# Performance work log

Measured on AMD Instinct MI355X. Metric: run time of the kernel, lower is better.

## Reference

```python
import jax, jax.numpy as jnp
import numpy as np

DIM = 1024
HEADS = 16
HEAD_DIM = DIM // HEADS  # 64
EPS = 1e-5


def layer_norm(x, w, b):
    # LayerNorm over last dim (head_dim), matching nn.LayerNorm defaults
    mu = jnp.mean(x, axis=-1, keepdims=True)
    var = jnp.mean(jnp.square(x - mu), axis=-1, keepdims=True)
    return (x - mu) * jax.lax.rsqrt(var + EPS) * w + b


def apply_rotary_emb(x, freqs):
    # x: [B, S, H, D]; freqs: [S, D/2] angles. Interleaved (complex) rotary:
    # pairs (x[2i], x[2i+1]) rotated by angle freqs[:, i].
    x1 = x[..., 0::2]
    x2 = x[..., 1::2]
    cos = jnp.cos(freqs)[None, :, None, :]
    sin = jnp.sin(freqs)[None, :, None, :]
    r1 = x1 * cos - x2 * sin
    r2 = x1 * sin + x2 * cos
    return jnp.stack([r1, r2], axis=-1).reshape(x.shape)


def setup_inputs() -> dict:
    key = jax.random.key(0)
    ks = jax.random.split(key, 8)
    B, S = 2, 2048
    x = jax.random.normal(ks[0], (B, S, DIM), dtype=jnp.float32)
    freqs = jax.random.uniform(ks[1], (S, HEAD_DIM // 2), dtype=jnp.float32)
    sc = 1.0 / np.sqrt(DIM)
    w_qkv = jax.random.normal(ks[2], (DIM, 4 * DIM), dtype=jnp.float32) * sc
    w_out = jax.random.normal(ks[3], (DIM, DIM), dtype=jnp.float32) * sc
    qn_w = jnp.ones((HEAD_DIM,), jnp.float32)
    qn_b = jnp.zeros((HEAD_DIM,), jnp.float32)
    kn_w = jnp.ones((HEAD_DIM,), jnp.float32)
    kn_b = jnp.zeros((HEAD_DIM,), jnp.float32)
    return {"x": x, "freqs": freqs, "w_qkv": w_qkv, "w_out": w_out,
            "qn_w": qn_w, "qn_b": qn_b, "kn_w": kn_w, "kn_b": kn_b}


def reference(x, freqs, w_qkv, w_out, qn_w, qn_b, kn_w, kn_b):
    B, S, _ = x.shape
    qkv = x @ w_qkv  # [B, S, 4*DIM]
    q, k, v, gate = jnp.split(qkv, 4, axis=-1)
    q = q.reshape(B, S, HEADS, HEAD_DIM)
    k = k.reshape(B, S, HEADS, HEAD_DIM)
    v = v.reshape(B, S, HEADS, HEAD_DIM)
    q = layer_norm(q, qn_w, qn_b)
    k = layer_norm(k, kn_w, kn_b)
    q = apply_rotary_emb(q, freqs)
    k = apply_rotary_emb(k, freqs)
    # flash_attn_func: non-causal softmax attention, scale 1/sqrt(head_dim)
    scale = 1.0 / np.sqrt(HEAD_DIM)
    scores = jnp.einsum('bqhd,bkhd->bhqk', q, k) * scale
    probs = jax.nn.softmax(scores, axis=-1)
    o = jnp.einsum('bhqk,bkhd->bqhd', probs, v)
    o = o.reshape(B, S, DIM)
    o = o * jax.nn.sigmoid(gate)
    return o @ w_out
```

## Files before the change

### kernel.cpp

```cpp
#include <hip/hip_runtime.h>


typedef _Float16 f16;
typedef _Float16 f16x8 __attribute__((ext_vector_type(8)));
typedef _Float16 f16x4 __attribute__((ext_vector_type(4)));
typedef float    f32x4 __attribute__((ext_vector_type(4)));

#define MFMA16(a, b, c) __builtin_amdgcn_mfma_f32_16x16x32_f16((a), (b), (c), 0, 0, 0)

__device__ __forceinline__ void gload16(const void* g, void* l) {
  __builtin_amdgcn_global_load_lds(
      (const __attribute__((address_space(1))) void*)g,
      (__attribute__((address_space(3))) void*)l, 16, 0, 0);
}

__device__ __forceinline__ float exp2_fast(float x) {
#if __has_builtin(__builtin_amdgcn_exp2f)
  return __builtin_amdgcn_exp2f(x);
#else
  float r;
  asm("v_exp_f32 %0, %1" : "=v"(r) : "v"(x));
  return r;
#endif
}
__device__ __forceinline__ unsigned pkrtz(float a, float b) {
  typedef __fp16 hf16x2 __attribute__((ext_vector_type(2)));
  union { hf16x2 h; unsigned u; } c;
  c.h = __builtin_amdgcn_cvt_pkrtz(a, b);
  return c.u;
}

__global__ void rope_table_kernel(const float* __restrict__ freqs, float* __restrict__ tbl) {
  int i = blockIdx.x * 256 + threadIdx.x;
  if (i >= 2048 * 32) return;
  int s = i >> 5, j = i & 31;
  float f = freqs[i];
  tbl[s * 64 + j]      = cosf(f);
  tbl[s * 64 + 32 + j] = sinf(f);
}

__global__ void cast_f16_kernel(const float* __restrict__ in, f16* __restrict__ out, int n8) {
  int i = blockIdx.x * 256 + threadIdx.x;
  if (i >= n8) return;
  float4 a = ((const float4*)in)[2 * i];
  float4 b = ((const float4*)in)[2 * i + 1];
  f16x8 o;
  o[0] = (f16)a.x; o[1] = (f16)a.y; o[2] = (f16)a.z; o[3] = (f16)a.w;
  o[4] = (f16)b.x; o[5] = (f16)b.y; o[6] = (f16)b.z; o[7] = (f16)b.w;
  ((f16x8*)out)[i] = o;
}

__global__ void transpose_cast_kernel(const float* __restrict__ in, f16* __restrict__ out,
                                      int R, int C) {
  __shared__ float t[64][65];
  int c0 = blockIdx.x * 64, r0 = blockIdx.y * 64;
  int tx = threadIdx.x & 15, ty = threadIdx.x >> 4;
#pragma unroll
  for (int i = 0; i < 4; ++i) {
    float4 v = *(const float4*)&in[(size_t)(r0 + ty + 16 * i) * C + c0 + tx * 4];
    t[ty + 16 * i][tx * 4 + 0] = v.x;
    t[ty + 16 * i][tx * 4 + 1] = v.y;
    t[ty + 16 * i][tx * 4 + 2] = v.z;
    t[ty + 16 * i][tx * 4 + 3] = v.w;
  }
  __syncthreads();
#pragma unroll
  for (int i = 0; i < 4; ++i) {
    int n = c0 + ty + 16 * i;
    int k = r0 + tx * 4;
    f16x4 o;
    o[0] = (f16)t[tx * 4 + 0][ty + 16 * i];
    o[1] = (f16)t[tx * 4 + 1][ty + 16 * i];
    o[2] = (f16)t[tx * 4 + 2][ty + 16 * i];
    o[3] = (f16)t[tx * 4 + 3][ty + 16 * i];
    *(f16x4*)&out[(size_t)n * R + k] = o;
  }
}

__global__ void fill_debug_kernel(float* out, int n) {
  int i = blockIdx.x * 256 + threadIdx.x;
  if (i < n) out[i] = 12345.0f;
}

__global__ __launch_bounds__(512, 1) void gemm_qkv_256(
    const f16* __restrict__ A, const f16* __restrict__ B, int K,
    f16* __restrict__ qraw, f16* __restrict__ kraw,
    f16* __restrict__ g16, f16* __restrict__ v_t) {
  __shared__ f16 sA[2][256 * 64], sB[2][256 * 64];
  const int tid = threadIdx.x, lane = tid & 63;
  const int wave = tid >> 6;
  const int wm = wave >> 2, wn = wave & 3;
  const int lg = lane >> 4, lr = lane & 15;
  const int n0 = blockIdx.x * 256, m0 = blockIdx.y * 256;

  auto stg = [&](int k0, int p) {
#pragma unroll
    for (int r = 0; r < 4; ++r) {
      int off = (tid + r * 512) * 16;
      int row = off >> 7;
      int col = ((off & 127) ^ ((row & 7) << 4)) >> 1;
      gload16(A + (size_t)(m0 + row) * K + k0 + col, (char*)sA[p] + off);
      gload16(B + (size_t)(n0 + row) * K + k0 + col, (char*)sB[p] + off);
    }
  };

  f32x4 acc[8][4];
#pragma unroll
  for (int m = 0; m < 8; ++m)
#pragma unroll
    for (int n = 0; n < 4; ++n) acc[m][n] = (f32x4){0.f, 0.f, 0.f, 0.f};

  stg(0, 0);
  const int NT = K >> 6;
  int cur = 0;
  for (int t = 0; t < NT; ++t, cur ^= 1) {
    __syncthreads();
    if (t + 1 < NT) stg((t + 1) << 6, cur ^ 1);
#pragma unroll
    for (int ks = 0; ks < 2; ++ks) {
      f16x8 bfr[4];
#pragma unroll
      for (int n = 0; n < 4; ++n) {
        int row = wn * 64 + n * 16 + lr;
        int boff = (row << 7) + (ks << 6) + (lg << 4);
        boff ^= (row & 7) << 4;
        bfr[n] = *(const f16x8*)((const char*)sB[cur] + boff);
      }
#pragma unroll
      for (int m = 0; m < 8; ++m) {
        int row = wm * 128 + m * 16 + lr;
        int aoff = (row << 7) + (ks << 6) + (lg << 4);
        aoff ^= (row & 7) << 4;
        f16x8 afr = *(const f16x8*)((const char*)sA[cur] + aoff);
#pragma unroll
        for (int n = 0; n < 4; ++n) acc[m][n] = MFMA16(afr, bfr[n], acc[m][n]);
      }
    }
  }

  const int region = n0 >> 10;
  if (region == 2) {
#pragma unroll
    for (int m = 0; m < 8; ++m) {
      int row = m0 + wm * 128 + m * 16 + 4 * lg;
#pragma unroll
      for (int n = 0; n < 4; ++n) {
        int c = (n0 & 1023) + wn * 64 + n * 16 + lr;
        int hh = c >> 6, d = c & 63;
        int bb = row >> 11, s = row & 2047;
        f16x4 pv;
        pv[0] = (f16)acc[m][n][0];
        pv[1] = (f16)acc[m][n][1];
        pv[2] = (f16)acc[m][n][2];
        pv[3] = (f16)acc[m][n][3];
        *(f16x4*)&v_t[(size_t)((bb * 16 + hh) * 64 + d) * 2048 + s] = pv;
      }
    }
  } else if (region == 3) {
#pragma unroll
    for (int m = 0; m < 8; ++m) {
      int row = m0 + wm * 128 + m * 16 + 4 * lg;
#pragma unroll
      for (int n = 0; n < 4; ++n) {
        int col = (n0 & 1023) + wn * 64 + n * 16 + lr;
#pragma unroll
        for (int r = 0; r < 4; ++r) {
          float sg = 1.0f / (1.0f + exp2_fast(acc[m][n][r] * -1.44269504f));
          g16[(size_t)(row + r) * 1024 + col] = (f16)sg;
        }
      }
    }
  } else {
    f16* dst = region ? kraw : qraw;
#pragma unroll
    for (int m = 0; m < 8; ++m) {
      int row = m0 + wm * 128 + m * 16 + 4 * lg;
#pragma unroll
      for (int n = 0; n < 4; ++n) {
        int col = (n0 & 1023) + wn * 64 + n * 16 + lr;
#pragma unroll
        for (int r = 0; r < 4; ++r)
          dst[(size_t)(row + r) * 1024 + col] = (f16)acc[m][n][r];
      }
    }
  }
}

__global__ __launch_bounds__(256, 2) void gemm_out_128x64(
    const f16* __restrict__ A, const f16* __restrict__ B,
    float* __restrict__ Cout, int M, int N, int K) {
  __shared__ f16 sA[2][128 * 64], sB[2][64 * 64];
  const int tid = threadIdx.x, lane = tid & 63;
  const int wave = tid >> 6, wm = wave >> 1, wn = wave & 1;
  const int lg = lane >> 4, lr = lane & 15;
  const int n0 = blockIdx.x * 64, m0 = blockIdx.y * 128;

  auto stg = [&](int k0, int p) {
#pragma unroll
    for (int r = 0; r < 4; ++r) {
      int off = (tid + r * 256) * 16;
      int row = off >> 7;
      int col = ((off & 127) ^ ((row & 7) << 4)) >> 1;
      gload16(A + (size_t)(m0 + row) * K + k0 + col, (char*)sA[p] + off);
    }
#pragma unroll
    for (int r = 0; r < 2; ++r) {
      int off = (tid + r * 256) * 16;
      int row = off >> 7;
      int col = ((off & 127) ^ ((row & 7) << 4)) >> 1;
      gload16(B + (size_t)(n0 + row) * K + k0 + col, (char*)sB[p] + off);
    }
  };

  f32x4 acc[4][2];
#pragma unroll
  for (int m = 0; m < 4; ++m)
#pragma unroll
    for (int n = 0; n < 2; ++n) acc[m][n] = (f32x4){0.f, 0.f, 0.f, 0.f};

  stg(0, 0);
  const int NT = K >> 6;
  int cur = 0;
  for (int t = 0; t < NT; ++t, cur ^= 1) {
    __syncthreads();
    if (t + 1 < NT) stg((t + 1) << 6, cur ^ 1);
#pragma unroll
    for (int ks = 0; ks < 2; ++ks) {
      f16x8 bfr[2];
#pragma unroll
      for (int n = 0; n < 2; ++n) {
        int row = wn * 32 + n * 16 + lr;
        int boff = (row << 7) + (ks << 6) + (lg << 4);
        boff ^= (row & 7) << 4;
        bfr[n] = *(const f16x8*)((const char*)sB[cur] + boff);
      }
#pragma unroll
      for (int m = 0; m < 4; ++m) {
        int row = wm * 64 + m * 16 + lr;
        int aoff = (row << 7) + (ks << 6) + (lg << 4);
        aoff ^= (row & 7) << 4;
        f16x8 afr = *(const f16x8*)((const char*)sA[cur] + aoff);
#pragma unroll
        for (int n = 0; n < 2; ++n) acc[m][n] = MFMA16(afr, bfr[n], acc[m][n]);
      }
    }
  }

#pragma unroll
  for (int m = 0; m < 4; ++m) {
    int row = m0 + wm * 64 + m * 16 + 4 * lg;
#pragma unroll
    for (int n = 0; n < 2; ++n) {
      int col = n0 + wn * 32 + n * 16 + lr;
#pragma unroll
      for (int r = 0; r < 4; ++r) Cout[(size_t)(row + r) * N + col] = acc[m][n][r];
    }
  }
}

__global__ void norm_k16_kernel(const f16* __restrict__ kr, const float* __restrict__ tbl,
                                const float* __restrict__ kn_w, const float* __restrict__ kn_b,
                                f16* __restrict__ k_h) {
  int row = blockIdx.x;
  int s = row & 2047;
  int hh = threadIdx.x >> 4, sub = threadIdx.x & 15;
  int base = row * 1024 + hh * 64 + sub * 4;
  float c0 = tbl[s * 64 + sub * 2 + 0], c1 = tbl[s * 64 + sub * 2 + 1];
  float s0 = tbl[s * 64 + 32 + sub * 2 + 0], s1 = tbl[s * 64 + 32 + sub * 2 + 1];
  f16x4 xr = *(const f16x4*)&kr[base];
  float x0 = (float)xr[0], x1 = (float)xr[1], x2 = (float)xr[2], x3 = (float)xr[3];
  float sum = x0 + x1 + x2 + x3;
  sum += __shfl_xor(sum, 1); sum += __shfl_xor(sum, 2);
  sum += __shfl_xor(sum, 4); sum += __shfl_xor(sum, 8);
  float mu = sum * (1.0f / 64.0f);
  float d0 = x0 - mu, d1 = x1 - mu, d2 = x2 - mu, d3 = x3 - mu;
  float sq = d0 * d0 + d1 * d1 + d2 * d2 + d3 * d3;
  sq += __shfl_xor(sq, 1); sq += __shfl_xor(sq, 2);
  sq += __shfl_xor(sq, 4); sq += __shfl_xor(sq, 8);
  float rstd = rsqrtf(sq * (1.0f / 64.0f) + 1e-5f);
  float4 w = *(const float4*)&kn_w[sub * 4];
  float4 bb = *(const float4*)&kn_b[sub * 4];
  float n0 = d0 * rstd * w.x + bb.x;
  float n1 = d1 * rstd * w.y + bb.y;
  float n2 = d2 * rstd * w.z + bb.z;
  float n3 = d3 * rstd * w.w + bb.w;
  float r0 = n0 * c0 - n1 * s0, r1 = n0 * s0 + n1 * c0;
  float r2 = n2 * c1 - n3 * s1, r3 = n2 * s1 + n3 * c1;
  f16x4 ov;
  ov[0] = (f16)r0; ov[1] = (f16)r1; ov[2] = (f16)r2; ov[3] = (f16)r3;
  *(f16x4*)&k_h[base] = ov;
}

__global__ __launch_bounds__(256, 2) void attn_kernel(const f16* __restrict__ qraw,
                                                      const f16* __restrict__ k_h,
                                                      const f16* __restrict__ v_t,
                                                      const float* __restrict__ tbl,
                                                      const float* __restrict__ qn_w,
                                                      const float* __restrict__ qn_b,
                                                      const f16* __restrict__ g16,
                                                      f16* __restrict__ a16) {
  __shared__ __align__(16) char smem[65536];
  const int tid = threadIdx.x, lane = tid & 63, wave = tid >> 6;
  const int lg = lane >> 4, lr = lane & 15;
  const int bh = blockIdx.x >> 4, qt = blockIdx.x & 15;
  const int b = bh >> 4, h = bh & 15;
  const int qrow0 = b * 2048 + qt * 128 + wave * 32;

  auto stage = [&](int kv0, int p) {
    char* kb = smem + p * 16384;
    char* vb = smem + 32768 + p * 16384;
#pragma unroll
    for (int r = 0; r < 4; ++r) {
      int off = (tid + r * 256) * 16;
      {
        int row = off >> 7;
        int col = ((off & 127) ^ ((row & 7) << 4)) >> 1;
        int g = ((row >> 5) << 5) + (((row >> 2) & 3) << 3) + (((row >> 4) & 1) << 2) + (row & 3);
        gload16(&k_h[(size_t)(b * 2048 + kv0 + g) * 1024 + h * 64 + col], kb + off);
      }
      {
        int d = off >> 8;
        int col = ((off & 255) ^ ((d & 15) << 4)) >> 1;
        gload16(&v_t[(size_t)(bh * 64 + d) * 2048 + kv0 + col], vb + off);
      }
    }
  };

  stage(0, 0);

  float wv[16], bv[16];
#pragma unroll
  for (int ks = 0; ks < 2; ++ks) {
    float4 wa = *(const float4*)&qn_w[ks * 32 + lg * 8];
    float4 wb = *(const float4*)&qn_w[ks * 32 + lg * 8 + 4];
    float4 ba = *(const float4*)&qn_b[ks * 32 + lg * 8];
    float4 bbv = *(const float4*)&qn_b[ks * 32 + lg * 8 + 4];
    wv[ks * 8 + 0] = wa.x; wv[ks * 8 + 1] = wa.y; wv[ks * 8 + 2] = wa.z; wv[ks * 8 + 3] = wa.w;
    wv[ks * 8 + 4] = wb.x; wv[ks * 8 + 5] = wb.y; wv[ks * 8 + 6] = wb.z; wv[ks * 8 + 7] = wb.w;
    bv[ks * 8 + 0] = ba.x; bv[ks * 8 + 1] = ba.y; bv[ks * 8 + 2] = ba.z; bv[ks * 8 + 3] = ba.w;
    bv[ks * 8 + 4] = bbv.x; bv[ks * 8 + 5] = bbv.y; bv[ks * 8 + 6] = bbv.z; bv[ks * 8 + 7] = bbv.w;
  }

  f16x8 qf[2][2];
#pragma unroll
  for (int n = 0; n < 2; ++n) {
    int row = qrow0 + n * 16 + lr;
    f16x8 raw[2];
    raw[0] = *(const f16x8*)&qraw[(size_t)row * 1024 + h * 64 + lg * 8];
    raw[1] = *(const f16x8*)&qraw[(size_t)row * 1024 + h * 64 + 32 + lg * 8];
    float x[16];
#pragma unroll
    for (int ks = 0; ks < 2; ++ks)
#pragma unroll
      for (int j = 0; j < 8; ++j) x[ks * 8 + j] = (float)raw[ks][j];
    float sum = 0.f;
#pragma unroll
    for (int i = 0; i < 16; ++i) sum += x[i];
    sum += __shfl_xor(sum, 16);
    sum += __shfl_xor(sum, 32);
    float mu = sum * (1.0f / 64.0f);
    float sq = 0.f;
#pragma unroll
    for (int i = 0; i < 16; ++i) { float d = x[i] - mu; sq += d * d; }
    sq += __shfl_xor(sq, 16);
    sq += __shfl_xor(sq, 32);
    float rstd = rsqrtf(sq * (1.0f / 64.0f) + 1e-5f);
    int srow = row & 2047;
    const float* tb = tbl + srow * 64;
#pragma unroll
    for (int ks = 0; ks < 2; ++ks) {
      float4 c4 = *(const float4*)&tb[ks * 16 + lg * 4];
      float4 s4 = *(const float4*)&tb[32 + ks * 16 + lg * 4];
      float cc[4] = {c4.x, c4.y, c4.z, c4.w};
      float ss[4] = {s4.x, s4.y, s4.z, s4.w};
      f16x8 o;
#pragma unroll
      for (int jj = 0; jj < 4; ++jj) {
        float y0 = (x[ks * 8 + 2 * jj] - mu) * rstd * wv[ks * 8 + 2 * jj] + bv[ks * 8 + 2 * jj];
        float y1 = (x[ks * 8 + 2 * jj + 1] - mu) * rstd * wv[ks * 8 + 2 * jj + 1] + bv[ks * 8 + 2 * jj + 1];
        o[2 * jj]     = (f16)(y0 * cc[jj] - y1 * ss[jj]);
        o[2 * jj + 1] = (f16)(y0 * ss[jj] + y1 * cc[jj]);
      }
      qf[n][ks] = o;
    }
  }

  f16x8 ones;
#pragma unroll
  for (int j = 0; j < 8; ++j) ones[j] = (f16)1.0f;

  f32x4 accO[4][2];
#pragma unroll
  for (int m = 0; m < 4; ++m) {
    accO[m][0] = (f32x4){0.f, 0.f, 0.f, 0.f};
    accO[m][1] = (f32x4){0.f, 0.f, 0.f, 0.f};
  }
  f32x4 accL[2] = {(f32x4){0.f, 0.f, 0.f, 0.f}, (f32x4){0.f, 0.f, 0.f, 0.f}};
  float mrun[2] = {-1e30f, -1e30f};
  const float SCL2 = 0.125f * 1.44269504f;
  const float THRP = 44.36f;
  const f32x4 fz = (f32x4){0.f, 0.f, 0.f, 0.f};

  int cur = 0;
  for (int t = 0; t < 16; ++t, cur ^= 1) {
    __syncthreads();
    if (t < 15) stage((t + 1) * 128, cur ^ 1);

    const char* kb = smem + cur * 16384;
    const char* vb = smem + 32768 + cur * 16384;

    f32x4 st[8][2];
    __builtin_amdgcn_s_setprio(1);
#pragma unroll
    for (int m = 0; m < 8; ++m) {
      int row = m * 16 + lr;
      int koff0 = ((row << 7) + (lg << 4)) ^ ((row & 7) << 4);
      int koff1 = ((row << 7) + 64 + (lg << 4)) ^ ((row & 7) << 4);
      f16x8 a0 = *(const f16x8*)(kb + koff0);
      f16x8 a1 = *(const f16x8*)(kb + koff1);
      st[m][0] = MFMA16(a1, qf[0][1], MFMA16(a0, qf[0][0], fz));
      st[m][1] = MFMA16(a1, qf[1][1], MFMA16(a0, qf[1][0], fz));
    }
    __builtin_amdgcn_s_setprio(0);

    uint2 pdw[2][8];
#pragma unroll
    for (int n = 0; n < 2; ++n) {
      float t03 = fmaxf(fmaxf(fmaxf(st[0][n][0], st[0][n][1]), fmaxf(st[0][n][2], st[0][n][3])),
                        fmaxf(fmaxf(st[1][n][0], st[1][n][1]), fmaxf(st[1][n][2], st[1][n][3])));
      float t47 = fmaxf(fmaxf(fmaxf(st[2][n][0], st[2][n][1]), fmaxf(st[2][n][2], st[2][n][3])),
                        fmaxf(fmaxf(st[3][n][0], st[3][n][1]), fmaxf(st[3][n][2], st[3][n][3])));
      float t8b = fmaxf(fmaxf(fmaxf(st[4][n][0], st[4][n][1]), fmaxf(st[4][n][2], st[4][n][3])),
                        fmaxf(fmaxf(st[5][n][0], st[5][n][1]), fmaxf(st[5][n][2], st[5][n][3])));
      float tcf = fmaxf(fmaxf(fmaxf(st[6][n][0], st[6][n][1]), fmaxf(st[6][n][2], st[6][n][3])),
                        fmaxf(fmaxf(st[7][n][0], st[7][n][1]), fmaxf(st[7][n][2], st[7][n][3])));
      float vm = fmaxf(fmaxf(t03, t47), fmaxf(t8b, tcf));
      vm = fmaxf(vm, __shfl_xor(vm, 16));
      vm = fmaxf(vm, __shfl_xor(vm, 32));
      if (__any(vm > mrun[n] + THRP)) {
        float mnew = fmaxf(mrun[n], vm);
        float fac = exp2_fast((mrun[n] - mnew) * SCL2);
        mrun[n] = mnew;
        accL[n] *= fac;
#pragma unroll
        for (int m = 0; m < 4; ++m) accO[m][n] *= fac;
      }
      float mc = mrun[n] * SCL2;
#pragma unroll
      for (int m = 0; m < 8; ++m) {
        float p0 = exp2_fast(st[m][n][0] * SCL2 - mc);
        float p1 = exp2_fast(st[m][n][1] * SCL2 - mc);
        float p2 = exp2_fast(st[m][n][2] * SCL2 - mc);
        float p3 = exp2_fast(st[m][n][3] * SCL2 - mc);
        pdw[n][m].x = pkrtz(p0, p1);
        pdw[n][m].y = pkrtz(p2, p3);
      }
    }

    f16x8 pb[2][4];
#pragma unroll
    for (int n = 0; n < 2; ++n)
#pragma unroll
      for (int ks = 0; ks < 4; ++ks) {
        union { uint4 u; f16x8 h; } c;
        c.u = make_uint4(pdw[n][2 * ks].x, pdw[n][2 * ks].y,
                         pdw[n][2 * ks + 1].x, pdw[n][2 * ks + 1].y);
        pb[n][ks] = c.h;
      }
    __builtin_amdgcn_s_setprio(1);
#pragma unroll
    for (int m = 0; m < 4; ++m)
#pragma unroll
      for (int ks = 0; ks < 4; ++ks) {
        int d = m * 16 + lr;
        int voff = (d << 8) + (ks << 6) + (lg << 4);
        voff ^= (d & 15) << 4;
        f16x8 av = *(const f16x8*)(vb + voff);
        accO[m][0] = MFMA16(av, pb[0][ks], accO[m][0]);
        accO[m][1] = MFMA16(av, pb[1][ks], accO[m][1]);
      }
#pragma unroll
    for (int ks = 0; ks < 4; ++ks) {
      accL[0] = MFMA16(ones, pb[0][ks], accL[0]);
      accL[1] = MFMA16(ones, pb[1][ks], accL[1]);
    }
    __builtin_amdgcn_s_setprio(0);
  }

#pragma unroll
  for (int n = 0; n < 2; ++n) {
    float rl = 1.0f / accL[n][0];
    int orow = qrow0 + n * 16 + lr;
#pragma unroll
    for (int m = 0; m < 4; ++m) {
      size_t idx = (size_t)orow * 1024 + h * 64 + m * 16 + lg * 4;
      f16x4 gv = *(const f16x4*)&g16[idx];
      f16x4 ov;
      ov[0] = (f16)(accO[m][n][0] * rl * (float)gv[0]);
      ov[1] = (f16)(accO[m][n][1] * rl * (float)gv[1]);
      ov[2] = (f16)(accO[m][n][2] * rl * (float)gv[2]);
      ov[3] = (f16)(accO[m][n][3] * rl * (float)gv[3]);
      *(f16x4*)&a16[idx] = ov;
    }
  }
}

extern "C" void kernel_launch(void* const* d_in, const int* in_sizes, int n_in,
                              void* d_out, int out_size, void* d_ws, size_t ws_size,
                              hipStream_t stream) {
  const float* x      = (const float*)d_in[0];
  const float* freqs  = (const float*)d_in[1];
  const float* w_qkv  = (const float*)d_in[2];
  const float* w_out  = (const float*)d_in[3];
  const float* qn_w   = (const float*)d_in[4];
  const float* qn_b   = (const float*)d_in[5];
  const float* kn_w   = (const float*)d_in[6];
  const float* kn_b   = (const float*)d_in[7];
  float* out = (float*)d_out;
  char* ws = (char*)d_ws;
  const size_t MB = 1024 * 1024;
  f16*   v_t   = (f16*)(ws + 0);
  f16*   x16   = (f16*)(ws + 8 * MB);
  f16*   wq16  = (f16*)(ws + 16 * MB);
  f16*   wo16  = (f16*)(ws + 24 * MB);
  f16*   qraw  = (f16*)(ws + 26 * MB);
  f16*   kraw  = (f16*)(ws + 34 * MB);
  f16*   k_h   = (f16*)(ws + 50 * MB);
  f16*   g16   = (f16*)(ws + 58 * MB);
  float* tbl   = (float*)(ws + 66 * MB);
  f16*   a16   = x16;

  if (ws_size < (size_t)67 * MB) {
    fill_debug_kernel<<<(out_size + 255) / 256, 256, 0, stream>>>(out, out_size);
    return;
  }

  rope_table_kernel<<<256, 256, 0, stream>>>(freqs, tbl);
  cast_f16_kernel<<<2048, 256, 0, stream>>>(x, x16, 524288);
  transpose_cast_kernel<<<dim3(64, 16), 256, 0, stream>>>(w_qkv, wq16, 1024, 4096);
  transpose_cast_kernel<<<dim3(16, 16), 256, 0, stream>>>(w_out, wo16, 1024, 1024);

  gemm_qkv_256<<<dim3(16, 16), 512, 0, stream>>>(x16, wq16, 1024, qraw, kraw, g16, v_t);
  norm_k16_kernel<<<4096, 256, 0, stream>>>(kraw, tbl, kn_w, kn_b, k_h);
  attn_kernel<<<512, 256, 0, stream>>>(qraw, k_h, v_t, tbl, qn_w, qn_b, g16, a16);
  gemm_out_128x64<<<dim3(16, 32), 256, 0, stream>>>(a16, wo16, out, 4096, 1024, 1024);
}
```

Baseline: 141.7 us.

## Replace double-buffered QKV GEMM staging with nine-slot LDS ring pipeline

The QKV projection GEMM now stages A and B tiles in 16KB units through a nine-slot shared-memory ring, issuing loads more than two k-steps ahead. Explicit vmcnt waits and raw barriers replace __syncthreads, and s_setprio is raised around the MFMA loop. The aim is to hide global-to-LDS load latency behind matrix math. The loop hardcodes K=1024 (16 steps), and the wait counts are tuned by hand, so a wrong count would cause a data race.

```diff
diff --git a/kernel.cpp b/kernel.cpp
--- a/kernel.cpp
+++ b/kernel.cpp
@@ -86,22 +86,34 @@
     const f16* __restrict__ A, const f16* __restrict__ B, int K,
     f16* __restrict__ qraw, f16* __restrict__ kraw,
     f16* __restrict__ g16, f16* __restrict__ v_t) {
-  __shared__ f16 sA[2][256 * 64], sB[2][256 * 64];
+  __shared__ f16 ring[9][8192];
   const int tid = threadIdx.x, lane = tid & 63;
   const int wave = tid >> 6;
   const int wm = wave >> 2, wn = wave & 3;
   const int lg = lane >> 4, lr = lane & 15;
   const int n0 = blockIdx.x * 256, m0 = blockIdx.y * 256;
-
-  auto stg = [&](int k0, int p) {
-#pragma unroll
-    for (int r = 0; r < 4; ++r) {
-      int off = (tid + r * 512) * 16;
-      int row = off >> 7;
-      int col = ((off & 127) ^ ((row & 7) << 4)) >> 1;
-      gload16(A + (size_t)(m0 + row) * K + k0 + col, (char*)sA[p] + off);
-      gload16(B + (size_t)(n0 + row) * K + k0 + col, (char*)sB[p] + off);
-    }
+  const f16* Abase = A + (size_t)m0 * K;
+  const f16* Bbase = B + (size_t)n0 * K;
+
+  int loff[2], grow[2], gcol[2];
+#pragma unroll
+  for (int r = 0; r < 2; ++r) {
+    int off = (tid + r * 512) * 16;
+    int rl = off >> 7;
+    loff[r] = off;
+    grow[r] = rl;
+    gcol[r] = ((off & 127) ^ ((rl & 7) << 4)) >> 1;
+  }
+
+  auto stage_unit = [&](int u) {
+    int t = u >> 2, j = u & 3;
+    char* dst = (char*)ring[u % 9];
+    const f16* src = (j < 2) ? Bbase : Abase;
+    int rbase = (j & 1) * 128;
+    int kb = t * 64;
+#pragma unroll
+    for (int r = 0; r < 2; ++r)
+      gload16(src + (size_t)(rbase + grow[r]) * K + kb + gcol[r], dst + loff[r]);
   };
 
   f32x4 acc[8][4];
@@ -110,33 +122,65 @@
 #pragma unroll
     for (int n = 0; n < 4; ++n) acc[m][n] = (f32x4){0.f, 0.f, 0.f, 0.f};
 
-  stg(0, 0);
-  const int NT = K >> 6;
-  int cur = 0;
-  for (int t = 0; t < NT; ++t, cur ^= 1) {
-    __syncthreads();
-    if (t + 1 < NT) stg((t + 1) << 6, cur ^ 1);
+  auto compute = [&](int t) {
+    const char* pB = (const char*)ring[(4 * t + (wn >> 1)) % 9];
+    const char* pA = (const char*)ring[(4 * t + 2 + wm) % 9];
+    const int rBb = (wn & 1) * 64;
 #pragma unroll
     for (int ks = 0; ks < 2; ++ks) {
       f16x8 bfr[4];
 #pragma unroll
       for (int n = 0; n < 4; ++n) {
-        int row = wn * 64 + n * 16 + lr;
-        int boff = (row << 7) + (ks << 6) + (lg << 4);
-        boff ^= (row & 7) << 4;
-        bfr[n] = *(const f16x8*)((const char*)sB[cur] + boff);
-      }
+        int rloc = rBb + n * 16 + lr;
+        int boff = (rloc << 7) + (ks << 6) + (lg << 4);
+        boff ^= (rloc & 7) << 4;
+        bfr[n] = *(const f16x8*)(pB + boff);
+      }
+      __builtin_amdgcn_s_setprio(1);
 #pragma unroll
       for (int m = 0; m < 8; ++m) {
-        int row = wm * 128 + m * 16 + lr;
-        int aoff = (row << 7) + (ks << 6) + (lg << 4);
-        aoff ^= (row & 7) << 4;
-        f16x8 afr = *(const f16x8*)((const char*)sA[cur] + aoff);
+        int rloc = m * 16 + lr;
+        int aoff = (rloc << 7) + (ks << 6) + (lg << 4);
+        aoff ^= (rloc & 7) << 4;
+        f16x8 afr = *(const f16x8*)(pA + aoff);
 #pragma unroll
         for (int n = 0; n < 4; ++n) acc[m][n] = MFMA16(afr, bfr[n], acc[m][n]);
       }
-    }
-  }
+      __builtin_amdgcn_s_setprio(0);
+    }
+  };
+
+#define WAITBAR(NSTR)                                        \
+  asm volatile("s_waitcnt vmcnt(" NSTR ")" ::: "memory");    \
+  __builtin_amdgcn_sched_barrier(0);                         \
+  __builtin_amdgcn_s_barrier();                              \
+  asm volatile("" ::: "memory");                             \
+  __builtin_amdgcn_sched_barrier(0);
+
+#define BARRIER2()                                           \
+  __builtin_amdgcn_sched_barrier(0);                         \
+  __builtin_amdgcn_s_barrier();                              \
+  asm volatile("" ::: "memory");                             \
+  __builtin_amdgcn_sched_barrier(0);
+
+  for (int u = 0; u < 9; ++u) stage_unit(u);
+
+  for (int t = 0; t < 16; ++t) {
+    if (t < 14) {
+      WAITBAR("10")
+    } else if (t == 14) {
+      WAITBAR("8")
+    } else {
+      WAITBAR("0")
+    }
+    compute(t);
+    BARRIER2()
+    int u0 = 4 * t + 9;
+    int ue = (u0 + 4 > 64) ? 64 : u0 + 4;
+    for (int u = u0; u < ue; ++u) stage_unit(u);
+  }
+#undef WAITBAR
+#undef BARRIER2
 
   const int region = n0 >> 10;
   if (region == 2) {
```

Result: slower. 168.5 us (+18.9%).
